# Performance work log

Hardware: AMD Instinct MI355X
Metric: run time of the kernel (lower is better)

## Reference

```python
import jax, jax.numpy as jnp
import numpy as np

NUM_NODES = 12
HEADS = 4
PERIOD = 24
HID = 144  # nn.LSTM(12*12, 12*12, 2)
NEG_INF = -9e15

ADJ = np.array([
    [1,0,0,0,0,1,0,0,0,0,1,1],
    [0,1,0,0,0,0,0,1,0,0,1,0],
    [0,0,1,0,0,0,1,0,0,0,0,1],
    [0,0,0,1,0,0,1,0,0,0,0,0],
    [0,0,0,0,1,1,0,0,0,0,0,0],
    [1,0,0,0,1,1,0,0,0,0,0,0],
    [0,0,1,1,0,0,1,0,0,0,1,0],
    [0,1,0,0,0,0,0,1,0,1,0,0],
    [0,0,0,0,0,0,0,0,1,1,1,1],
    [0,0,0,0,0,0,0,1,1,1,1,0],
    [1,1,0,0,0,0,1,0,1,1,1,1],
    [1,0,1,0,0,0,0,0,1,0,1,1]], dtype=np.int32)
EI, EJ = np.nonzero(ADJ)  # static edge list (row-major order, matches torch nonzero)


def gat_layer(x, W, b, a):
    # x: [B, N, c_in]; W: [c_in, H*c]; a: [H, 2c]
    B, N, _ = x.shape
    H = a.shape[0]
    h = (x @ W + b).reshape(B, N, H, -1)  # [B,N,H,c]
    # NOTE: adj has batch dim 1 in the original, so logits come from sample 0 only
    hi = h[0, EI]  # [E,H,c]
    hj = h[0, EJ]
    logits = jnp.einsum('ehc,hc->eh', jnp.concatenate([hi, hj], axis=-1), a)
    logits = jax.nn.leaky_relu(logits, 0.2)
    mat = jnp.full((N, N, H), NEG_INF, dtype=logits.dtype).at[EI, EJ].set(logits)
    probs = jax.nn.softmax(mat, axis=1)  # softmax over j (dim=2 in torch incl. batch)
    out = jnp.einsum('ijh,bjhc->bihc', probs, h)  # broadcast attn over batch
    return out.reshape(B, N, -1)  # concat heads


def lstm2(x, params, h0, c0):
    # x: [T,B,D]; params: list of (Wih,Whh,bih,bhh); h0,c0: [L,B,HID]
    hs, cs = [], []
    y = x
    for l, (Wih, Whh, bih, bhh) in enumerate(params):
        def step(carry, xt, Wih=Wih, Whh=Whh, bih=bih, bhh=bhh):
            h, c = carry
            g = xt @ Wih.T + h @ Whh.T + (bih + bhh)
            i, f, gg, o = jnp.split(g, 4, axis=-1)  # torch gate order i,f,g,o
            c2 = jax.nn.sigmoid(f) * c + jax.nn.sigmoid(i) * jnp.tanh(gg)
            h2 = jax.nn.sigmoid(o) * jnp.tanh(c2)
            return (h2, c2), h2
        (hT, cT), y = jax.lax.scan(step, (h0[l], c0[l]), y)
        hs.append(hT)
        cs.append(cT)
    return y, jnp.stack(hs), jnp.stack(cs)


def reference(x, gW0, gb0, ga0, gW1, gb1, ga1,
              eWih0, eWhh0, ebih0, ebhh0, eWih1, eWhh1, ebih1, ebhh1,
              dWih0, dWhh0, dbih0, dbhh0, dWih1, dWhh1, dbih1, dbhh1,
              gW3, gb3, ga3, gW4, gb4, ga4, fW, fb):
    B = x.shape[0]
    h = jax.nn.elu(gat_layer(x, gW0, gb0, ga0))           # [B,12,16]
    h = jax.nn.elu(gat_layer(h, gW1, gb1, ga1))           # [B,12,12]
    seq = h.reshape(PERIOD, -1, NUM_NODES * 12)            # [24, B/24, 144]
    Bb = seq.shape[1]
    z = jnp.zeros((2, Bb, HID), dtype=seq.dtype)
    enc_params = [(eWih0, eWhh0, ebih0, ebhh0), (eWih1, eWhh1, ebih1, ebhh1)]
    dec_params = [(dWih0, dWhh0, dbih0, dbhh0), (dWih1, dWhh1, dbih1, dbhh1)]
    y, hn, _ = lstm2(seq, enc_params, z, z)
    dec_in = jnp.zeros_like(y)
    y, _, _ = lstm2(dec_in, dec_params, hn, jnp.zeros_like(hn))
    h = y.reshape(-1, NUM_NODES, 12)                       # [B,12,12]
    h = jax.nn.elu(gat_layer(h, gW3, gb3, ga3))            # [B,12,16]
    h = jax.nn.elu(gat_layer(h, gW4, gb4, ga4))            # [B,12,24]
    h = h.reshape(B, NUM_NODES * 24)
    h = jax.nn.leaky_relu(h @ fW + fb, 0.01)               # fc_layers
    xr = h.reshape(B, NUM_NODES, -1)                       # [B,12,22]
    # F.mse_loss(..., reduce='sum') -> legacy truthy reduce => mean reduction
    out = jnp.mean((x - xr) ** 2, axis=(1, 2)).reshape(-1, 1)
    return out


def setup_inputs() -> dict:
    key = jax.random.key(0)
    ks = iter(jax.random.split(key, 64))
    def p(shape, s=0.2):
        return s * jax.random.normal(next(ks), shape, dtype=jnp.float32)
    B = 98304  # multiple of period=24
    d = {
        'x': jax.random.normal(next(ks), (B, 12, 22), dtype=jnp.float32),
        'gW0': p((22, 16)), 'gb0': p((16,)), 'ga0': p((4, 8)),
        'gW1': p((16, 12)), 'gb1': p((12,)), 'ga1': p((4, 6)),
    }
    for pre in ('e', 'd'):
        for l in (0, 1):
            d[f'{pre}Wih{l}'] = p((576, 144))
            d[f'{pre}Whh{l}'] = p((576, 144))
            d[f'{pre}bih{l}'] = p((576,))
            d[f'{pre}bhh{l}'] = p((576,))
    d.update({'gW3': p((12, 16)), 'gb3': p((16,)), 'ga3': p((4, 8)),
              'gW4': p((16, 24)), 'gb4': p((24,)), 'ga4': p((4, 12)),
              'fW': p((288, 264)), 'fb': p((264,))})
    return d
```

## Files before the change

### kernel.cpp

```cpp
#include <hip/hip_runtime.h>

#define DI __device__ __forceinline__

typedef short bfrag8 __attribute__((ext_vector_type(8)));
typedef float ffrag4 __attribute__((ext_vector_type(4)));

DI ushort f2b(float f){
  union { float f; unsigned u; } v; v.f = f;
  unsigned u = v.u;
  u += 0x7FFF + ((u >> 16) & 1);
  return (ushort)(u >> 16);
}
DI float b2f(ushort h){
  union { unsigned u; float f; } v; v.u = ((unsigned)h) << 16;
  return v.f;
}
DI float sigm(float x){ return 1.0f / (1.0f + __expf(-x)); }
DI float tanh_(float x){ return 1.0f - 2.0f / (1.0f + __expf(2.0f * x)); }
DI float elu_(float x){ return x > 0.f ? x : __expf(x) - 1.f; }

__global__ void k_probs(const float* xf, const ushort* xb, int in_c,
                        const float* W1, const float* b1, const float* a1, int hc1, int c1,
                        const float* W2, const float* b2, const float* a2, int hc2, int c2,
                        float* outA, float* outB)
{
  __shared__ float xs[12 * 22];
  __shared__ float h1[12 * 16];
  __shared__ float lg[4 * 144];
  __shared__ float pr[4 * 144];
  __shared__ float h1e[12 * 16];
  __shared__ float h2[12 * 24];
  const int t = threadIdx.x;
  const unsigned adj[12] = {0xC21u,0x482u,0x844u,0x048u,0x030u,0x031u,
                            0x44Cu,0x282u,0xF00u,0x780u,0xF43u,0xD05u};
  if (t < 12 * in_c){
    if (xf) xs[t] = xf[t];
    else    xs[t] = b2f(xb[t]);
  }
  __syncthreads();
  if (t < 12 * hc1){
    int i = t / hc1, o = t % hc1;
    float v = b1[o];
    for (int k = 0; k < in_c; k++) v += xs[i * in_c + k] * W1[k * hc1 + o];
    h1[t] = v;
  }
  __syncthreads();
  {
    int h = t / 144, ij = t % 144, i = ij / 12, j = ij % 12;
    float v;
    if ((adj[i] >> j) & 1){
      v = 0.f;
      for (int c = 0; c < c1; c++)
        v += a1[h*2*c1 + c] * h1[i*hc1 + h*c1 + c] + a1[h*2*c1 + c1 + c] * h1[j*hc1 + h*c1 + c];
      v = v > 0.f ? v : 0.2f * v;
    } else v = -9e15f;
    lg[t] = v;
  }
  __syncthreads();
  if (t < 48){
    int h = t / 12, i = t % 12;
    const float* row = &lg[h*144 + i*12];
    float m = row[0];
    for (int j = 1; j < 12; j++) m = fmaxf(m, row[j]);
    float e[12], s = 0.f;
    for (int j = 0; j < 12; j++){ e[j] = __expf(row[j] - m); s += e[j]; }
    float inv = 1.f / s;
    for (int j = 0; j < 12; j++){
      float p = e[j] * inv;
      pr[h*144 + i*12 + j] = p;
      outA[h*144 + i*12 + j] = p;
    }
  }
  __syncthreads();
  if (t < 12 * hc1){
    int i = t / hc1, o = t % hc1, h = o / c1;
    float v = 0.f;
    for (int j = 0; j < 12; j++) v += pr[h*144 + i*12 + j] * h1[j*hc1 + o];
    h1e[t] = elu_(v);
  }
  __syncthreads();
  if (t < 12 * hc2){
    int i = t / hc2, o = t % hc2;
    float v = b2[o];
    for (int k = 0; k < hc1; k++) v += h1e[i*hc1 + k] * W2[k*hc2 + o];
    h2[t] = v;
  }
  __syncthreads();
  {
    int h = t / 144, ij = t % 144, i = ij / 12, j = ij % 12;
    float v;
    if ((adj[i] >> j) & 1){
      v = 0.f;
      for (int c = 0; c < c2; c++)
        v += a2[h*2*c2 + c] * h2[i*hc2 + h*c2 + c] + a2[h*2*c2 + c2 + c] * h2[j*hc2 + h*c2 + c];
      v = v > 0.f ? v : 0.2f * v;
    } else v = -9e15f;
    lg[t] = v;
  }
  __syncthreads();
  if (t < 48){
    int h = t / 12, i = t % 12;
    const float* row = &lg[h*144 + i*12];
    float m = row[0];
    for (int j = 1; j < 12; j++) m = fmaxf(m, row[j]);
    float e[12], s = 0.f;
    for (int j = 0; j < 12; j++){ e[j] = __expf(row[j] - m); s += e[j]; }
    float inv = 1.f / s;
    for (int j = 0; j < 12; j++) outB[h*144 + i*12 + j] = e[j] * inv;
  }
}

__global__ void k_prep_op(const float* __restrict__ W, const float* __restrict__ p,
                          int Cin, int Cout, int hdiv, int K, int KT, int N,
                          ushort* __restrict__ dst)
{
  int bI = blockIdx.x;
  int kt = bI % KT, nt = bI / KT;
  int l = threadIdx.x, ln = l & 15, q = l >> 4;
  int n = nt * 16 + ln;
  for (int j = 0; j < 8; j++){
    int k = kt * 32 + q * 8 + j;
    float v = 0.f;
    if (k < K && n < N){
      if (p){
        int jj = k / Cin, kk = k % Cin;
        int i = n / Cout, o = n % Cout;
        v = p[(o / hdiv) * 144 + i * 12 + jj] * W[kk * Cout + o];
      } else {
        v = W[k * Cout + n];
      }
    }
    dst[((long)bI * 64 + l) * 8 + j] = f2b(v);
  }
}

__global__ void k_prep_lstm(const float* eWih0, const float* eWhh0,
                            const float* eWih1, const float* eWhh1,
                            const float* dWhh0,
                            const float* dWih1, const float* dWhh1,
                            ushort* __restrict__ dstBase)
{
  int combo = blockIdx.y;
  const float* Wh; const float* Wx; long off; int ntau;
  if (combo == 0){ Wh = eWhh0; Wx = eWih0; off = 0;      ntau = 72; }
  else if (combo == 1){ Wh = eWhh1; Wx = eWih1; off = 184320; ntau = 72; }
  else if (combo == 2){ Wh = dWhh0; Wx = dWhh0; off = 368640; ntau = 36; }
  else { Wh = dWhh1; Wx = dWih1; off = 460800; ntau = 72; }
  int bI = blockIdx.x;
  int tau = bI / 5, kt = bI % 5;
  if (tau >= ntau) return;
  const float* W = (tau < 36) ? Wh : Wx;
  int tt = (tau < 36) ? tau : tau - 36;
  int gt = tt / 9, ct = tt % 9;
  int l = threadIdx.x, ln = l & 15, q = l >> 4;
  int n = gt * 144 + ct * 16 + ln;
  ushort* d = dstBase + off;
  for (int j = 0; j < 8; j++){
    int k = kt * 32 + q * 8 + j;
    float v = (k < 144) ? W[(long)n * 144 + k] : 0.f;
    d[((long)bI * 64 + l) * 8 + j] = f2b(v);
  }
}

__global__ __launch_bounds__(512) void k_gat01(
    const float* __restrict__ x, const ushort* __restrict__ M0f, const float* __restrict__ b0,
    const ushort* __restrict__ M1f, const float* __restrict__ b1,
    ushort* __restrict__ seq)
{
  __shared__ ushort xs[128 * 288];
  __shared__ ushort h1e[128 * 200];
  int t = threadIdx.x;
  long row0 = (long)blockIdx.x * 128;
  int w = t >> 6, l = t & 63, q = l >> 4, ln = l & 15;
  if (t < 384){
    int row = t / 3, seg = t % 3;
    *(uint4*)&xs[row * 288 + 264 + seg * 8] = make_uint4(0u, 0u, 0u, 0u);
  }
  for (int idx = t; idx < 8448; idx += 512){
    int row = idx / 66, c4 = idx % 66;
    float4 v = *(const float4*)&x[(row0 + row) * 264 + c4 * 4];
    ushort4 o; o.x = f2b(v.x); o.y = f2b(v.y); o.z = f2b(v.z); o.w = f2b(v.w);
    *(ushort4*)&xs[row * 288 + c4 * 4] = o;
  }
  int nta[2] = {w, (w < 4) ? 8 + w : -1};
  bfrag8 f0[2][9];
  #pragma unroll
  for (int ii = 0; ii < 2; ii++)
    if (nta[ii] >= 0)
      #pragma unroll
      for (int kt = 0; kt < 9; kt++)
        f0[ii][kt] = *(const bfrag8*)&M0f[((long)(nta[ii] * 9 + kt) * 64 + l) * 8];
  float bias0 = b0[ln];
  __syncthreads();
  for (int rb = 0; rb < 8; rb++){
    bfrag8 af[9];
    #pragma unroll
    for (int kt = 0; kt < 9; kt++)
      af[kt] = *(const bfrag8*)&xs[(rb * 16 + ln) * 288 + kt * 32 + q * 8];
    #pragma unroll
    for (int ii = 0; ii < 2; ii++){
      if (nta[ii] < 0) continue;
      ffrag4 acc = {bias0, bias0, bias0, bias0};
      #pragma unroll
      for (int kt = 0; kt < 9; kt++)
        acc = __builtin_amdgcn_mfma_f32_16x16x32_bf16(af[kt], f0[ii][kt], acc, 0, 0, 0);
      #pragma unroll
      for (int r = 0; r < 4; r++)
        h1e[(rb * 16 + q * 4 + r) * 200 + nta[ii] * 16 + ln] = f2b(elu_(acc[r]));
    }
  }
  int ntb[2] = {w, (w == 0) ? 8 : -1};
  bfrag8 f1[2][6];
  #pragma unroll
  for (int ii = 0; ii < 2; ii++)
    if (ntb[ii] >= 0)
      #pragma unroll
      for (int kt = 0; kt < 6; kt++)
        f1[ii][kt] = *(const bfrag8*)&M1f[((long)(ntb[ii] * 6 + kt) * 64 + l) * 8];
  __syncthreads();
  for (int rb = 0; rb < 8; rb++){
    bfrag8 af[6];
    #pragma unroll
    for (int kt = 0; kt < 6; kt++)
      af[kt] = *(const bfrag8*)&h1e[(rb * 16 + ln) * 200 + kt * 32 + q * 8];
    #pragma unroll
    for (int ii = 0; ii < 2; ii++){
      if (ntb[ii] < 0) continue;
      int n = ntb[ii] * 16 + ln;
      float bias = b1[n % 12];
      ffrag4 acc = {bias, bias, bias, bias};
      #pragma unroll
      for (int kt = 0; kt < 6; kt++)
        acc = __builtin_amdgcn_mfma_f32_16x16x32_bf16(af[kt], f1[ii][kt], acc, 0, 0, 0);
      #pragma unroll
      for (int r = 0; r < 4; r++)
        xs[(rb * 16 + q * 4 + r) * 144 + n] = f2b(elu_(acc[r]));
    }
  }
  __syncthreads();
  for (int i = t; i < 2304; i += 512)
    *(uint4*)&seq[row0 * 144 + (long)i * 8] = *(uint4*)&xs[i * 8];
}

template<bool HASX>
__global__ __launch_bounds__(512, 2) void k_scan(
    const ushort* __restrict__ Wf,
    const ushort* __restrict__ seqin,
    const float* __restrict__ bih, const float* __restrict__ bhh,
    const ushort* __restrict__ h0,
    ushort* __restrict__ Y,
    ushort* __restrict__ hT)
{
  __shared__ float Px[2][11520];
  __shared__ float P8[1280];
  __shared__ ushort hl[2][2688];
  int t = threadIdx.x, rbk = blockIdx.x;
  int w = t >> 6, l = t & 63, q = l >> 4, ln = l & 15;
  if (t < 336){
    int row = t / 21, ch = t % 21;
    uint4 z = make_uint4(0u, 0u, 0u, 0u);
    if (h0 && ch < 18) z = *(const uint4*)&h0[((long)rbk * 16 + row) * 144 + ch * 8];
    *(uint4*)&hl[0][row * 168 + ch * 8] = z;
    *(uint4*)&hl[1][row * 168 + ch * 8] = make_uint4(0u, 0u, 0u, 0u);
  }
  if (w < 4){
    bfrag8 wh[2][4][5], w8[5];
    #pragma unroll
    for (int ci = 0; ci < 2; ci++)
      #pragma unroll
      for (int gt = 0; gt < 4; gt++)
        #pragma unroll
        for (int kt = 0; kt < 5; kt++)
          wh[ci][gt][kt] = *(const bfrag8*)&Wf[((long)((gt * 9 + 2 * w + ci) * 5 + kt) * 64 + l) * 8];
    #pragma unroll
    for (int kt = 0; kt < 5; kt++)
      w8[kt] = *(const bfrag8*)&Wf[((long)((w * 9 + 8) * 5 + kt) * 64 + l) * 8];
    float cst[2][4] = {};
    float c8 = 0.f;
    __syncthreads();
    for (int ts = 0; ts < 24; ts++){
      int par = ts & 1;
      const ushort* hlr = &hl[par][0];
      ushort* hlw = &hl[par ^ 1][0];
      bfrag8 ah[5];
      #pragma unroll
      for (int kt = 0; kt < 5; kt++)
        ah[kt] = *(const bfrag8*)&hlr[ln * 168 + kt * 32 + q * 8];
      #pragma unroll
      for (int ci = 0; ci < 2; ci++){
        int ct = 2 * w + ci;
        ffrag4 acc[4];
        #pragma unroll
        for (int gt = 0; gt < 4; gt++)
          acc[gt] = *(ffrag4*)&Px[par][(gt * 144 + ct * 16 + ln) * 20 + q * 4];
        #pragma unroll
        for (int gt = 0; gt < 4; gt++)
          #pragma unroll
          for (int kt = 0; kt < 5; kt++)
            acc[gt] = __builtin_amdgcn_mfma_f32_16x16x32_bf16(ah[kt], wh[ci][gt][kt], acc[gt], 0, 0, 0);
        #pragma unroll
        for (int r = 0; r < 4; r++){
          float cn = sigm(acc[1][r]) * cst[ci][r] + sigm(acc[0][r]) * tanh_(acc[2][r]);
          cst[ci][r] = cn;
          ushort hb = f2b(sigm(acc[3][r]) * tanh_(cn));
          hlw[(q * 4 + r) * 168 + ct * 16 + ln] = hb;
          if (Y) Y[(((long)ts * 4096) + rbk * 16 + q * 4 + r) * 144 + ct * 16 + ln] = hb;
        }
      }
      {
        ffrag4 a8 = *(ffrag4*)&Px[par][(w * 144 + 128 + ln) * 20 + q * 4];
        #pragma unroll
        for (int kt = 0; kt < 5; kt++)
          a8 = __builtin_amdgcn_mfma_f32_16x16x32_bf16(ah[kt], w8[kt], a8, 0, 0, 0);
        *(ffrag4*)&P8[(w * 16 + ln) * 20 + q * 4] = a8;
      }
      __syncthreads();
      if (t < 256){
        int row = t >> 4, c8c = t & 15;
        float iv = P8[(0 * 16 + c8c) * 20 + row];
        float fv = P8[(1 * 16 + c8c) * 20 + row];
        float gv = P8[(2 * 16 + c8c) * 20 + row];
        float ov = P8[(3 * 16 + c8c) * 20 + row];
        float cn = sigm(fv) * c8 + sigm(iv) * tanh_(gv);
        c8 = cn;
        ushort hb = f2b(sigm(ov) * tanh_(cn));
        hl[par ^ 1][row * 168 + 128 + c8c] = hb;
        if (Y) Y[(((long)ts * 4096) + rbk * 16 + row) * 144 + 128 + c8c] = hb;
      }
      __syncthreads();
    }
  } else {
    int j = w - 4;
    bfrag8 wx[9][5];
    float biasx[9];
    #pragma unroll
    for (int i = 0; i < 9; i++){
      int n = j * 144 + i * 16 + ln;
      biasx[i] = bih[n] + bhh[n];
      if (HASX)
        #pragma unroll
        for (int kt = 0; kt < 5; kt++)
          wx[i][kt] = *(const bfrag8*)&Wf[((long)((36 + j * 9 + i) * 5 + kt) * 64 + l) * 8];
    }
    bfrag8 axc[5];
    if (HASX){
      const ushort* xr = &seqin[((long)rbk * 16 + ln) * 144];
      #pragma unroll
      for (int kt = 0; kt < 5; kt++)
        axc[kt] = *(const bfrag8*)&xr[kt * 32 + q * 8];
      #pragma unroll
      for (int i = 0; i < 9; i++){
        ffrag4 acc = {biasx[i], biasx[i], biasx[i], biasx[i]};
        #pragma unroll
        for (int kt = 0; kt < 5; kt++)
          acc = __builtin_amdgcn_mfma_f32_16x16x32_bf16(axc[kt], wx[i][kt], acc, 0, 0, 0);
        *(ffrag4*)&Px[0][(j * 144 + i * 16 + ln) * 20 + q * 4] = acc;
      }
      const ushort* xr1 = &seqin[(4096L + (long)rbk * 16 + ln) * 144];
      #pragma unroll
      for (int kt = 0; kt < 5; kt++)
        axc[kt] = *(const bfrag8*)&xr1[kt * 32 + q * 8];
    } else {
      #pragma unroll
      for (int i = 0; i < 9; i++){
        ffrag4 acc = {biasx[i], biasx[i], biasx[i], biasx[i]};
        *(ffrag4*)&Px[0][(j * 144 + i * 16 + ln) * 20 + q * 4] = acc;
        *(ffrag4*)&Px[1][(j * 144 + i * 16 + ln) * 20 + q * 4] = acc;
      }
    }
    __syncthreads();
    for (int ts = 0; ts < 24; ts++){
      if (HASX && ts < 23){
        int par = ts & 1;
        #pragma unroll
        for (int i = 0; i < 9; i++){
          ffrag4 acc = {biasx[i], biasx[i], biasx[i], biasx[i]};
          #pragma unroll
          for (int kt = 0; kt < 5; kt++)
            acc = __builtin_amdgcn_mfma_f32_16x16x32_bf16(axc[kt], wx[i][kt], acc, 0, 0, 0);
          *(ffrag4*)&Px[par ^ 1][(j * 144 + i * 16 + ln) * 20 + q * 4] = acc;
        }
        if (ts < 22){
          const ushort* xr = &seqin[(((long)(ts + 2)) * 4096 + (long)rbk * 16 + ln) * 144];
          #pragma unroll
          for (int kt = 0; kt < 5; kt++)
            axc[kt] = *(const bfrag8*)&xr[kt * 32 + q * 8];
        }
      }
      __syncthreads();
      __syncthreads();
    }
  }
  if (hT && t < 288){
    int row = t / 18, ch = t % 18;
    *(uint4*)&hT[((long)rbk * 16 + row) * 144 + ch * 8] = *(uint4*)&hl[0][row * 168 + ch * 8];
  }
}

__global__ __launch_bounds__(512) void k_tail(
    const ushort* __restrict__ Ya, const ushort* __restrict__ M3f, const float* __restrict__ b3,
    const ushort* __restrict__ M4f, const float* __restrict__ b4,
    const ushort* __restrict__ fWt, const float* __restrict__ fb,
    const float* __restrict__ x, float* __restrict__ out)
{
  __shared__ ushort h3e[128 * 200];
  __shared__ ushort bufB[128 * 288];
  __shared__ float psum[128 * 8];
  ushort* ys = bufB;
  ushort* h4e = bufB;
  int t = threadIdx.x;
  long row0 = (long)blockIdx.x * 128;
  int w = t >> 6, l = t & 63, q = l >> 4, ln = l & 15;
  if (t < 256){
    int row = t / 2, seg = t % 2;
    *(uint4*)&ys[row * 160 + 144 + seg * 8] = make_uint4(0u, 0u, 0u, 0u);
  }
  for (int idx = t; idx < 2304; idx += 512){
    int row = idx / 18, ch = idx % 18;
    *(uint4*)&ys[row * 160 + ch * 8] = *(const uint4*)&Ya[(row0 + row) * 144 + (long)ch * 8];
  }
  int nta[2] = {w, (w < 4) ? 8 + w : -1};
  bfrag8 f3[2][5];
  #pragma unroll
  for (int ii = 0; ii < 2; ii++)
    if (nta[ii] >= 0)
      #pragma unroll
      for (int kt = 0; kt < 5; kt++)
        f3[ii][kt] = *(const bfrag8*)&M3f[((long)(nta[ii] * 5 + kt) * 64 + l) * 8];
  float bias3 = b3[ln];
  __syncthreads();
  for (int rb = 0; rb < 8; rb++){
    bfrag8 af[5];
    #pragma unroll
    for (int kt = 0; kt < 5; kt++)
      af[kt] = *(const bfrag8*)&ys[(rb * 16 + ln) * 160 + kt * 32 + q * 8];
    #pragma unroll
    for (int ii = 0; ii < 2; ii++){
      if (nta[ii] < 0) continue;
      ffrag4 acc = {bias3, bias3, bias3, bias3};
      #pragma unroll
      for (int kt = 0; kt < 5; kt++)
        acc = __builtin_amdgcn_mfma_f32_16x16x32_bf16(af[kt], f3[ii][kt], acc, 0, 0, 0);
      #pragma unroll
      for (int r = 0; r < 4; r++)
        h3e[(rb * 16 + q * 4 + r) * 200 + nta[ii] * 16 + ln] = f2b(elu_(acc[r]));
    }
  }
  int ntb[3] = {2 * w, 2 * w + 1, (w < 2) ? 16 + w : -1};
  bfrag8 f4[3][6];
  #pragma unroll
  for (int ii = 0; ii < 3; ii++)
    if (ntb[ii] >= 0)
      #pragma unroll
      for (int kt = 0; kt < 6; kt++)
        f4[ii][kt] = *(const bfrag8*)&M4f[((long)(ntb[ii] * 6 + kt) * 64 + l) * 8];
  __syncthreads();
  for (int rb = 0; rb < 8; rb++){
    bfrag8 af[6];
    #pragma unroll
    for (int kt = 0; kt < 6; kt++)
      af[kt] = *(const bfrag8*)&h3e[(rb * 16 + ln) * 200 + kt * 32 + q * 8];
    #pragma unroll
    for (int ii = 0; ii < 3; ii++){
      if (ntb[ii] < 0) continue;
      int n = ntb[ii] * 16 + ln;
      float bias = b4[n % 24];
      ffrag4 acc = {bias, bias, bias, bias};
      #pragma unroll
      for (int kt = 0; kt < 6; kt++)
        acc = __builtin_amdgcn_mfma_f32_16x16x32_bf16(af[kt], f4[ii][kt], acc, 0, 0, 0);
      #pragma unroll
      for (int r = 0; r < 4; r++)
        h4e[(rb * 16 + q * 4 + r) * 288 + n] = f2b(elu_(acc[r]));
    }
  }
  int ntc[3] = {2 * w, 2 * w + 1, (w == 0) ? 16 : -1};
  bfrag8 f5[3][9];
  float bias5[3] = {0.f, 0.f, 0.f};
  #pragma unroll
  for (int ii = 0; ii < 3; ii++)
    if (ntc[ii] >= 0){
      #pragma unroll
      for (int kt = 0; kt < 9; kt++)
        f5[ii][kt] = *(const bfrag8*)&fWt[((long)(ntc[ii] * 9 + kt) * 64 + l) * 8];
      int n = ntc[ii] * 16 + ln;
      bias5[ii] = (n < 264) ? fb[n] : 0.f;
    }
  __syncthreads();
  for (int rb = 0; rb < 8; rb++){
    bfrag8 af[9];
    #pragma unroll
    for (int kt = 0; kt < 9; kt++)
      af[kt] = *(const bfrag8*)&h4e[(rb * 16 + ln) * 288 + kt * 32 + q * 8];
    float s4[4] = {0.f, 0.f, 0.f, 0.f};
    #pragma unroll
    for (int ii = 0; ii < 3; ii++){
      if (ntc[ii] < 0) continue;
      ffrag4 acc = {bias5[ii], bias5[ii], bias5[ii], bias5[ii]};
      #pragma unroll
      for (int kt = 0; kt < 9; kt++)
        acc = __builtin_amdgcn_mfma_f32_16x16x32_bf16(af[kt], f5[ii][kt], acc, 0, 0, 0);
      int n = ntc[ii] * 16 + ln;
      if (n < 264){
        #pragma unroll
        for (int r = 0; r < 4; r++){
          float v = acc[r];
          v = v > 0.f ? v : 0.01f * v;
          long row = row0 + rb * 16 + q * 4 + r;
          float d = x[row * 264 + n] - v;
          s4[r] += d * d;
        }
      }
    }
    #pragma unroll
    for (int off = 1; off < 16; off <<= 1){
      #pragma unroll
      for (int r = 0; r < 4; r++) s4[r] += __shfl_xor(s4[r], off, 16);
    }
    if (ln == 0){
      #pragma unroll
      for (int r = 0; r < 4; r++) psum[(rb * 16 + q * 4 + r) * 8 + w] = s4[r];
    }
  }
  __syncthreads();
  if (t < 128){
    float s = 0.f;
    for (int k = 0; k < 8; k++) s += psum[t * 8 + k];
    out[row0 + t] = s * (1.0f / 264.0f);
  }
}

extern "C" void kernel_launch(void* const* d_in, const int* in_sizes, int n_in,
                              void* d_out, int out_size, void* d_ws, size_t ws_size,
                              hipStream_t stream)
{
  const float* x     = (const float*)d_in[0];
  const float* gW0   = (const float*)d_in[1];
  const float* gb0   = (const float*)d_in[2];
  const float* ga0   = (const float*)d_in[3];
  const float* gW1   = (const float*)d_in[4];
  const float* gb1   = (const float*)d_in[5];
  const float* ga1   = (const float*)d_in[6];
  const float* eWih0 = (const float*)d_in[7];
  const float* eWhh0 = (const float*)d_in[8];
  const float* ebih0 = (const float*)d_in[9];
  const float* ebhh0 = (const float*)d_in[10];
  const float* eWih1 = (const float*)d_in[11];
  const float* eWhh1 = (const float*)d_in[12];
  const float* ebih1 = (const float*)d_in[13];
  const float* ebhh1 = (const float*)d_in[14];
  const float* dWhh0 = (const float*)d_in[16];
  const float* dbih0 = (const float*)d_in[17];
  const float* dbhh0 = (const float*)d_in[18];
  const float* dWih1 = (const float*)d_in[19];
  const float* dWhh1 = (const float*)d_in[20];
  const float* dbih1 = (const float*)d_in[21];
  const float* dbhh1 = (const float*)d_in[22];
  const float* gW3   = (const float*)d_in[23];
  const float* gb3   = (const float*)d_in[24];
  const float* ga3   = (const float*)d_in[25];
  const float* gW4   = (const float*)d_in[26];
  const float* gb4   = (const float*)d_in[27];
  const float* ga4   = (const float*)d_in[28];
  const float* fW    = (const float*)d_in[29];
  const float* fb    = (const float*)d_in[30];

  char* ws = (char*)d_ws;
  float*  probs0 = (float*)(ws + 0);
  float*  probs1 = (float*)(ws + 2304);
  float*  probs3 = (float*)(ws + 4608);
  float*  probs4 = (float*)(ws + 6912);
  ushort* M0f    = (ushort*)(ws + 9216);
  ushort* M1f    = (ushort*)(ws + 119808);
  ushort* M3f    = (ushort*)(ws + 175104);
  ushort* M4f    = (ushort*)(ws + 236544);
  ushort* fWt    = (ushort*)(ws + 347136);
  ushort* lstmF  = (ushort*)(ws + 503808);
  ushort* seq    = (ushort*)(ws + 1794048);
  ushort* Ya     = (ushort*)(ws + 30105600);
  ushort* Yb     = (ushort*)(ws + 58417152);
  ushort* hT0    = (ushort*)(ws + 86728704);
  ushort* hT1    = (ushort*)(ws + 87908352);
  float* out = (float*)d_out;

  k_prep_lstm<<<dim3(360, 4), 64, 0, stream>>>(eWih0, eWhh0, eWih1, eWhh1,
                                               dWhh0, dWih1, dWhh1, lstmF);
  k_prep_op<<<153, 64, 0, stream>>>(fW, nullptr, 0, 264, 1, 288, 9, 264, fWt);
  k_probs<<<1, 576, 0, stream>>>(x, nullptr, 22,
                                 gW0, gb0, ga0, 16, 4,
                                 gW1, gb1, ga1, 12, 3,
                                 probs0, probs1);
  k_prep_op<<<108, 64, 0, stream>>>(gW0, probs0, 22, 16, 4, 264, 9, 192, M0f);
  k_prep_op<<<54, 64, 0, stream>>>(gW1, probs1, 16, 12, 3, 192, 6, 144, M1f);
  k_gat01<<<768, 512, 0, stream>>>(x, M0f, gb0, M1f, gb1, seq);

  k_scan<true><<<256, 512, 0, stream>>>(lstmF + 0L,      seq, ebih0, ebhh0, nullptr, Ya, hT0);
  k_scan<true><<<256, 512, 0, stream>>>(lstmF + 184320L, Ya, ebih1, ebhh1, nullptr, nullptr, hT1);
  k_scan<false><<<256, 512, 0, stream>>>(lstmF + 368640L, nullptr, dbih0, dbhh0, hT0, Yb, nullptr);
  k_scan<true><<<256, 512, 0, stream>>>(lstmF + 460800L, Yb, dbih1, dbhh1, hT1, Ya, nullptr);

  k_probs<<<1, 576, 0, stream>>>(nullptr, Ya, 12,
                                 gW3, gb3, ga3, 16, 4,
                                 gW4, gb4, ga4, 24, 6,
                                 probs3, probs4);
  k_prep_op<<<60, 64, 0, stream>>>(gW3, probs3, 12, 16, 4, 144, 5, 192, M3f);
  k_prep_op<<<108, 64, 0, stream>>>(gW4, probs4, 16, 24, 6, 192, 6, 288, M4f);
  k_tail<<<768, 512, 0, stream>>>(Ya, M3f, gb3, M4f, gb4, fWt, fb, x, out);
}
```

Measured before the change: 598.2 us.

## Fuse weight prep into fewer kernels, halve GAT tiles, restructure LSTM scan

Merges the LSTM and FC weight-prep kernels into one launch, and folds the GAT operator-matrix construction into k_probs, removing several small launches. The GAT head and tail kernels now process 64 rows per block (twice the blocks) with padded LDS strides to improve occupancy and reduce bank conflicts. The LSTM scan is reorganized so four waves compute all hidden-gate MFMAs into a shared Ph buffer while the other waves prefetch input projections, and all 512 threads then do the elementwise cell update and write Y with vectorized stores. This costs more LDS traffic and an extra barrier per timestep in exchange for spreading the gate math across all threads.

```diff
diff --git a/kernel.cpp b/kernel.cpp
--- a/kernel.cpp
+++ b/kernel.cpp
@@ -22,12 +22,14 @@
 __global__ void k_probs(const float* xf, const ushort* xb, int in_c,
                         const float* W1, const float* b1, const float* a1, int hc1, int c1,
                         const float* W2, const float* b2, const float* a2, int hc2, int c2,
-                        float* outA, float* outB)
+                        ushort* __restrict__ M1dst, int KT1,
+                        ushort* __restrict__ M2dst, int KT2)
 {
   __shared__ float xs[12 * 22];
   __shared__ float h1[12 * 16];
-  __shared__ float lg[4 * 144];
-  __shared__ float pr[4 * 144];
+  __shared__ float lg[576];
+  __shared__ float prA[576];
+  __shared__ float prB[576];
   __shared__ float h1e[12 * 16];
   __shared__ float h2[12 * 24];
   const int t = threadIdx.x;
@@ -65,17 +67,13 @@
     float e[12], s = 0.f;
     for (int j = 0; j < 12; j++){ e[j] = __expf(row[j] - m); s += e[j]; }
     float inv = 1.f / s;
-    for (int j = 0; j < 12; j++){
-      float p = e[j] * inv;
-      pr[h*144 + i*12 + j] = p;
-      outA[h*144 + i*12 + j] = p;
-    }
+    for (int j = 0; j < 12; j++) prA[h*144 + i*12 + j] = e[j] * inv;
   }
   __syncthreads();
   if (t < 12 * hc1){
     int i = t / hc1, o = t % hc1, h = o / c1;
     float v = 0.f;
-    for (int j = 0; j < 12; j++) v += pr[h*144 + i*12 + j] * h1[j*hc1 + o];
+    for (int j = 0; j < 12; j++) v += prA[h*144 + i*12 + j] * h1[j*hc1 + o];
     h1e[t] = elu_(v);
   }
   __syncthreads();
@@ -106,45 +104,81 @@
     float e[12], s = 0.f;
     for (int j = 0; j < 12; j++){ e[j] = __expf(row[j] - m); s += e[j]; }
     float inv = 1.f / s;
-    for (int j = 0; j < 12; j++) outB[h*144 + i*12 + j] = e[j] * inv;
-  }
-}
-
-__global__ void k_prep_op(const float* __restrict__ W, const float* __restrict__ p,
-                          int Cin, int Cout, int hdiv, int K, int KT, int N,
-                          ushort* __restrict__ dst)
+    for (int j = 0; j < 12; j++) prB[h*144 + i*12 + j] = e[j] * inv;
+  }
+  __syncthreads();
+  {
+    int NT = (12 * hc1) / 16, K = 12 * in_c;
+    for (int idx = t; idx < NT * KT1 * 64; idx += 576){
+      int bI = idx >> 6, li = idx & 63;
+      int kt = bI % KT1, nt = bI / KT1;
+      int n = nt * 16 + (li & 15);
+      int i = n / hc1, o = n % hc1;
+      union { ushort u[8]; uint4 v; } pk;
+      #pragma unroll
+      for (int j = 0; j < 8; j++){
+        int k = kt * 32 + (li >> 4) * 8 + j;
+        float v = 0.f;
+        if (k < K){
+          int jj = k / in_c, kk = k % in_c;
+          v = prA[(o / c1) * 144 + i * 12 + jj] * W1[kk * hc1 + o];
+        }
+        pk.u[j] = f2b(v);
+      }
+      *(uint4*)&M1dst[(long)idx * 8] = pk.v;
+    }
+  }
+  {
+    int NT = (12 * hc2) / 16, K = 12 * hc1;
+    for (int idx = t; idx < NT * KT2 * 64; idx += 576){
+      int bI = idx >> 6, li = idx & 63;
+      int kt = bI % KT2, nt = bI / KT2;
+      int n = nt * 16 + (li & 15);
+      int i = n / hc2, o = n % hc2;
+      union { ushort u[8]; uint4 v; } pk;
+      #pragma unroll
+      for (int j = 0; j < 8; j++){
+        int k = kt * 32 + (li >> 4) * 8 + j;
+        float v = 0.f;
+        if (k < K){
+          int jj = k / hc1, kk = k % hc1;
+          v = prB[(o / c2) * 144 + i * 12 + jj] * W2[kk * hc2 + o];
+        }
+        pk.u[j] = f2b(v);
+      }
+      *(uint4*)&M2dst[(long)idx * 8] = pk.v;
+    }
+  }
+}
+
+__global__ void k_prep_all(const float* eWih0, const float* eWhh0,
+                           const float* eWih1, const float* eWhh1,
+                           const float* dWhh0,
+                           const float* dWih1, const float* dWhh1,
+                           const float* fW,
+                           ushort* __restrict__ lstmF, ushort* __restrict__ fWt)
 {
-  int bI = blockIdx.x;
-  int kt = bI % KT, nt = bI / KT;
+  int y = blockIdx.y;
   int l = threadIdx.x, ln = l & 15, q = l >> 4;
-  int n = nt * 16 + ln;
-  for (int j = 0; j < 8; j++){
-    int k = kt * 32 + q * 8 + j;
-    float v = 0.f;
-    if (k < K && n < N){
-      if (p){
-        int jj = k / Cin, kk = k % Cin;
-        int i = n / Cout, o = n % Cout;
-        v = p[(o / hdiv) * 144 + i * 12 + jj] * W[kk * Cout + o];
-      } else {
-        v = W[k * Cout + n];
-      }
-    }
-    dst[((long)bI * 64 + l) * 8 + j] = f2b(v);
-  }
-}
-
-__global__ void k_prep_lstm(const float* eWih0, const float* eWhh0,
-                            const float* eWih1, const float* eWhh1,
-                            const float* dWhh0,
-                            const float* dWih1, const float* dWhh1,
-                            ushort* __restrict__ dstBase)
-{
-  int combo = blockIdx.y;
+  if (y == 4){
+    int bI = blockIdx.x;
+    if (bI >= 153) return;
+    int nt = bI / 9, kt = bI % 9;
+    int n = nt * 16 + ln;
+    union { ushort u[8]; uint4 v; } pk;
+    #pragma unroll
+    for (int j = 0; j < 8; j++){
+      int k = kt * 32 + q * 8 + j;
+      float v = (k < 288 && n < 264) ? fW[k * 264 + n] : 0.f;
+      pk.u[j] = f2b(v);
+    }
+    *(uint4*)&fWt[((long)(bI * 64 + l)) * 8] = pk.v;
+    return;
+  }
   const float* Wh; const float* Wx; long off; int ntau;
-  if (combo == 0){ Wh = eWhh0; Wx = eWih0; off = 0;      ntau = 72; }
-  else if (combo == 1){ Wh = eWhh1; Wx = eWih1; off = 184320; ntau = 72; }
-  else if (combo == 2){ Wh = dWhh0; Wx = dWhh0; off = 368640; ntau = 36; }
+  if (y == 0){ Wh = eWhh0; Wx = eWih0; off = 0;      ntau = 72; }
+  else if (y == 1){ Wh = eWhh1; Wx = eWih1; off = 184320; ntau = 72; }
+  else if (y == 2){ Wh = dWhh0; Wx = dWhh0; off = 368640; ntau = 36; }
   else { Wh = dWhh1; Wx = dWih1; off = 460800; ntau = 72; }
   int bI = blockIdx.x;
   int tau = bI / 5, kt = bI % 5;
@@ -152,14 +186,16 @@
   const float* W = (tau < 36) ? Wh : Wx;
   int tt = (tau < 36) ? tau : tau - 36;
   int gt = tt / 9, ct = tt % 9;
-  int l = threadIdx.x, ln = l & 15, q = l >> 4;
   int n = gt * 144 + ct * 16 + ln;
-  ushort* d = dstBase + off;
+  ushort* d = lstmF + off;
+  union { ushort u[8]; uint4 v; } pk;
+  #pragma unroll
   for (int j = 0; j < 8; j++){
     int k = kt * 32 + q * 8 + j;
     float v = (k < 144) ? W[(long)n * 144 + k] : 0.f;
-    d[((long)bI * 64 + l) * 8 + j] = f2b(v);
-  }
+    pk.u[j] = f2b(v);
+  }
+  *(uint4*)&d[((long)(bI * 64 + l)) * 8] = pk.v;
 }
 
 __global__ __launch_bounds__(512) void k_gat01(
@@ -167,20 +203,20 @@
     const ushort* __restrict__ M1f, const float* __restrict__ b1,
     ushort* __restrict__ seq)
 {
-  __shared__ ushort xs[128 * 288];
-  __shared__ ushort h1e[128 * 200];
+  __shared__ ushort xs[64 * 296];
+  __shared__ ushort h1e[64 * 200];
   int t = threadIdx.x;
-  long row0 = (long)blockIdx.x * 128;
+  long row0 = (long)blockIdx.x * 64;
   int w = t >> 6, l = t & 63, q = l >> 4, ln = l & 15;
-  if (t < 384){
-    int row = t / 3, seg = t % 3;
-    *(uint4*)&xs[row * 288 + 264 + seg * 8] = make_uint4(0u, 0u, 0u, 0u);
-  }
-  for (int idx = t; idx < 8448; idx += 512){
+  if (t < 256){
+    int row = t >> 2, seg = t & 3;
+    *(uint4*)&xs[row * 296 + 264 + seg * 8] = make_uint4(0u, 0u, 0u, 0u);
+  }
+  for (int idx = t; idx < 4224; idx += 512){
     int row = idx / 66, c4 = idx % 66;
     float4 v = *(const float4*)&x[(row0 + row) * 264 + c4 * 4];
     ushort4 o; o.x = f2b(v.x); o.y = f2b(v.y); o.z = f2b(v.z); o.w = f2b(v.w);
-    *(ushort4*)&xs[row * 288 + c4 * 4] = o;
+    *(ushort4*)&xs[row * 296 + c4 * 4] = o;
   }
   int nta[2] = {w, (w < 4) ? 8 + w : -1};
   bfrag8 f0[2][9];
@@ -192,11 +228,11 @@
         f0[ii][kt] = *(const bfrag8*)&M0f[((long)(nta[ii] * 9 + kt) * 64 + l) * 8];
   float bias0 = b0[ln];
   __syncthreads();
-  for (int rb = 0; rb < 8; rb++){
+  for (int rb = 0; rb < 4; rb++){
     bfrag8 af[9];
     #pragma unroll
     for (int kt = 0; kt < 9; kt++)
-      af[kt] = *(const bfrag8*)&xs[(rb * 16 + ln) * 288 + kt * 32 + q * 8];
+      af[kt] = *(const bfrag8*)&xs[(rb * 16 + ln) * 296 + kt * 32 + q * 8];
     #pragma unroll
     for (int ii = 0; ii < 2; ii++){
       if (nta[ii] < 0) continue;
@@ -218,7 +254,7 @@
       for (int kt = 0; kt < 6; kt++)
         f1[ii][kt] = *(const bfrag8*)&M1f[((long)(ntb[ii] * 6 + kt) * 64 + l) * 8];
   __syncthreads();
-  for (int rb = 0; rb < 8; rb++){
+  for (int rb = 0; rb < 4; rb++){
     bfrag8 af[6];
     #pragma unroll
     for (int kt = 0; kt < 6; kt++)
@@ -238,7 +274,7 @@
     }
   }
   __syncthreads();
-  for (int i = t; i < 2304; i += 512)
+  for (int i = t; i < 1152; i += 512)
     *(uint4*)&seq[row0 * 144 + (long)i * 8] = *(uint4*)&xs[i * 8];
 }
 
@@ -251,98 +287,38 @@
     ushort* __restrict__ Y,
     ushort* __restrict__ hT)
 {
+  __shared__ float Ph[11520];
   __shared__ float Px[2][11520];
-  __shared__ float P8[1280];
   __shared__ ushort hl[2][2688];
   int t = threadIdx.x, rbk = blockIdx.x;
   int w = t >> 6, l = t & 63, q = l >> 4, ln = l & 15;
   if (t < 336){
     int row = t / 21, ch = t % 21;
     uint4 z = make_uint4(0u, 0u, 0u, 0u);
+    *(uint4*)&hl[1][row * 168 + ch * 8] = z;
     if (h0 && ch < 18) z = *(const uint4*)&h0[((long)rbk * 16 + row) * 144 + ch * 8];
     *(uint4*)&hl[0][row * 168 + ch * 8] = z;
-    *(uint4*)&hl[1][row * 168 + ch * 8] = make_uint4(0u, 0u, 0u, 0u);
-  }
-  if (w < 4){
-    bfrag8 wh[2][4][5], w8[5];
-    #pragma unroll
-    for (int ci = 0; ci < 2; ci++)
-      #pragma unroll
-      for (int gt = 0; gt < 4; gt++)
-        #pragma unroll
-        for (int kt = 0; kt < 5; kt++)
-          wh[ci][gt][kt] = *(const bfrag8*)&Wf[((long)((gt * 9 + 2 * w + ci) * 5 + kt) * 64 + l) * 8];
-    #pragma unroll
-    for (int kt = 0; kt < 5; kt++)
-      w8[kt] = *(const bfrag8*)&Wf[((long)((w * 9 + 8) * 5 + kt) * 64 + l) * 8];
-    float cst[2][4] = {};
-    float c8 = 0.f;
-    __syncthreads();
-    for (int ts = 0; ts < 24; ts++){
-      int par = ts & 1;
-      const ushort* hlr = &hl[par][0];
-      ushort* hlw = &hl[par ^ 1][0];
-      bfrag8 ah[5];
+  }
+  bool isH = (w < 4);
+  bfrag8 wf[9][5];
+  if (HASX || isH){
+    #pragma unroll
+    for (int i = 0; i < 9; i++){
+      int tau = isH ? (w * 9 + i) : (36 + (w - 4) * 9 + i);
       #pragma unroll
       for (int kt = 0; kt < 5; kt++)
-        ah[kt] = *(const bfrag8*)&hlr[ln * 168 + kt * 32 + q * 8];
-      #pragma unroll
-      for (int ci = 0; ci < 2; ci++){
-        int ct = 2 * w + ci;
-        ffrag4 acc[4];
-        #pragma unroll
-        for (int gt = 0; gt < 4; gt++)
-          acc[gt] = *(ffrag4*)&Px[par][(gt * 144 + ct * 16 + ln) * 20 + q * 4];
-        #pragma unroll
-        for (int gt = 0; gt < 4; gt++)
-          #pragma unroll
-          for (int kt = 0; kt < 5; kt++)
-            acc[gt] = __builtin_amdgcn_mfma_f32_16x16x32_bf16(ah[kt], wh[ci][gt][kt], acc[gt], 0, 0, 0);
-        #pragma unroll
-        for (int r = 0; r < 4; r++){
-          float cn = sigm(acc[1][r]) * cst[ci][r] + sigm(acc[0][r]) * tanh_(acc[2][r]);
-          cst[ci][r] = cn;
-          ushort hb = f2b(sigm(acc[3][r]) * tanh_(cn));
-          hlw[(q * 4 + r) * 168 + ct * 16 + ln] = hb;
-          if (Y) Y[(((long)ts * 4096) + rbk * 16 + q * 4 + r) * 144 + ct * 16 + ln] = hb;
-        }
-      }
-      {
-        ffrag4 a8 = *(ffrag4*)&Px[par][(w * 144 + 128 + ln) * 20 + q * 4];
-        #pragma unroll
-        for (int kt = 0; kt < 5; kt++)
-          a8 = __builtin_amdgcn_mfma_f32_16x16x32_bf16(ah[kt], w8[kt], a8, 0, 0, 0);
-        *(ffrag4*)&P8[(w * 16 + ln) * 20 + q * 4] = a8;
-      }
-      __syncthreads();
-      if (t < 256){
-        int row = t >> 4, c8c = t & 15;
-        float iv = P8[(0 * 16 + c8c) * 20 + row];
-        float fv = P8[(1 * 16 + c8c) * 20 + row];
-        float gv = P8[(2 * 16 + c8c) * 20 + row];
-        float ov = P8[(3 * 16 + c8c) * 20 + row];
-        float cn = sigm(fv) * c8 + sigm(iv) * tanh_(gv);
-        c8 = cn;
-        ushort hb = f2b(sigm(ov) * tanh_(cn));
-        hl[par ^ 1][row * 168 + 128 + c8c] = hb;
-        if (Y) Y[(((long)ts * 4096) + rbk * 16 + row) * 144 + 128 + c8c] = hb;
-      }
-      __syncthreads();
-    }
-  } else {
-    int j = w - 4;
-    bfrag8 wx[9][5];
-    float biasx[9];
+        wf[i][kt] = *(const bfrag8*)&Wf[((long)(tau * 5 + kt) * 64 + l) * 8];
+    }
+  }
+  float cst[5] = {0.f, 0.f, 0.f, 0.f, 0.f};
+  float biasx[9];
+  bfrag8 axc[5];
+  if (!isH){
     #pragma unroll
     for (int i = 0; i < 9; i++){
-      int n = j * 144 + i * 16 + ln;
+      int n = ((w - 4) * 9 + i) * 16 + ln;
       biasx[i] = bih[n] + bhh[n];
-      if (HASX)
-        #pragma unroll
-        for (int kt = 0; kt < 5; kt++)
-          wx[i][kt] = *(const bfrag8*)&Wf[((long)((36 + j * 9 + i) * 5 + kt) * 64 + l) * 8];
-    }
-    bfrag8 axc[5];
+    }
     if (HASX){
       const ushort* xr = &seqin[((long)rbk * 16 + ln) * 144];
       #pragma unroll
@@ -353,8 +329,8 @@
         ffrag4 acc = {biasx[i], biasx[i], biasx[i], biasx[i]};
         #pragma unroll
         for (int kt = 0; kt < 5; kt++)
-          acc = __builtin_amdgcn_mfma_f32_16x16x32_bf16(axc[kt], wx[i][kt], acc, 0, 0, 0);
-        *(ffrag4*)&Px[0][(j * 144 + i * 16 + ln) * 20 + q * 4] = acc;
+          acc = __builtin_amdgcn_mfma_f32_16x16x32_bf16(axc[kt], wf[i][kt], acc, 0, 0, 0);
+        *(ffrag4*)&Px[0][(((w - 4) * 9 + i) * 16 + ln) * 20 + q * 4] = acc;
       }
       const ushort* xr1 = &seqin[(4096L + (long)rbk * 16 + ln) * 144];
       #pragma unroll
@@ -364,31 +340,64 @@
       #pragma unroll
       for (int i = 0; i < 9; i++){
         ffrag4 acc = {biasx[i], biasx[i], biasx[i], biasx[i]};
-        *(ffrag4*)&Px[0][(j * 144 + i * 16 + ln) * 20 + q * 4] = acc;
-        *(ffrag4*)&Px[1][(j * 144 + i * 16 + ln) * 20 + q * 4] = acc;
+        *(ffrag4*)&Px[0][(((w - 4) * 9 + i) * 16 + ln) * 20 + q * 4] = acc;
+        *(ffrag4*)&Px[1][(((w - 4) * 9 + i) * 16 + ln) * 20 + q * 4] = acc;
+      }
+    }
+  }
+  __syncthreads();
+  for (int ts = 0; ts < 24; ts++){
+    int par = ts & 1;
+    if (isH){
+      bfrag8 ah[5];
+      #pragma unroll
+      for (int kt = 0; kt < 5; kt++)
+        ah[kt] = *(const bfrag8*)&hl[par][ln * 168 + kt * 32 + q * 8];
+      #pragma unroll
+      for (int i = 0; i < 9; i++){
+        ffrag4 acc = {0.f, 0.f, 0.f, 0.f};
+        #pragma unroll
+        for (int kt = 0; kt < 5; kt++)
+          acc = __builtin_amdgcn_mfma_f32_16x16x32_bf16(ah[kt], wf[i][kt], acc, 0, 0, 0);
+        *(ffrag4*)&Ph[((w * 9 + i) * 16 + ln) * 20 + q * 4] = acc;
+      }
+    } else if (HASX && ts < 23){
+      #pragma unroll
+      for (int i = 0; i < 9; i++){
+        ffrag4 acc = {biasx[i], biasx[i], biasx[i], biasx[i]};
+        #pragma unroll
+        for (int kt = 0; kt < 5; kt++)
+          acc = __builtin_amdgcn_mfma_f32_16x16x32_bf16(axc[kt], wf[i][kt], acc, 0, 0, 0);
+        *(ffrag4*)&Px[par ^ 1][(((w - 4) * 9 + i) * 16 + ln) * 20 + q * 4] = acc;
+      }
+      if (ts < 22){
+        const ushort* xr = &seqin[(((long)(ts + 2)) * 4096 + (long)rbk * 16 + ln) * 144];
+        #pragma unroll
+        for (int kt = 0; kt < 5; kt++)
+          axc[kt] = *(const bfrag8*)&xr[kt * 32 + q * 8];
       }
     }
     __syncthreads();
-    for (int ts = 0; ts < 24; ts++){
-      if (HASX && ts < 23){
-        int par = ts & 1;
-        #pragma unroll
-        for (int i = 0; i < 9; i++){
-          ffrag4 acc = {biasx[i], biasx[i], biasx[i], biasx[i]};
-          #pragma unroll
-          for (int kt = 0; kt < 5; kt++)
-            acc = __builtin_amdgcn_mfma_f32_16x16x32_bf16(axc[kt], wx[i][kt], acc, 0, 0, 0);
-          *(ffrag4*)&Px[par ^ 1][(j * 144 + i * 16 + ln) * 20 + q * 4] = acc;
-        }
-        if (ts < 22){
-          const ushort* xr = &seqin[(((long)(ts + 2)) * 4096 + (long)rbk * 16 + ln) * 144];
-          #pragma unroll
-          for (int kt = 0; kt < 5; kt++)
-            axc[kt] = *(const bfrag8*)&xr[kt * 32 + q * 8];
-        }
-      }
-      __syncthreads();
-      __syncthreads();
+    #pragma unroll
+    for (int j = 0; j < 5; j++){
+      int cell = j * 512 + t;
+      if (cell < 2304){
+        int col = cell >> 4, row = cell & 15;
+        int a = col * 20 + row;
+        float iv = Ph[a]        + Px[par][a];
+        float fv = Ph[2880 + a] + Px[par][2880 + a];
+        float gv = Ph[5760 + a] + Px[par][5760 + a];
+        float ov = Ph[8640 + a] + Px[par][8640 + a];
+        float cn = sigm(fv) * cst[j] + sigm(iv) * tanh_(gv);
+        cst[j] = cn;
+        hl[par ^ 1][row * 168 + col] = f2b(sigm(ov) * tanh_(cn));
+      }
+    }
+    __syncthreads();
+    if (Y && t < 288){
+      int row = t / 18, ch = t % 18;
+      *(uint4*)&Y[(((long)ts * 4096) + rbk * 16 + row) * 144 + ch * 8] =
+          *(uint4*)&hl[par ^ 1][row * 168 + ch * 8];
     }
   }
   if (hT && t < 288){
@@ -403,21 +412,21 @@
     const ushort* __restrict__ fWt, const float* __restrict__ fb,
     const float* __restrict__ x, float* __restrict__ out)
 {
-  __shared__ ushort h3e[128 * 200];
-  __shared__ ushort bufB[128 * 288];
-  __shared__ float psum[128 * 8];
+  __shared__ ushort h3e[64 * 200];
+  __shared__ ushort bufB[64 * 296];
+  __shared__ float psum[64 * 8];
   ushort* ys = bufB;
   ushort* h4e = bufB;
   int t = threadIdx.x;
-  long row0 = (long)blockIdx.x * 128;
+  long row0 = (long)blockIdx.x * 64;
   int w = t >> 6, l = t & 63, q = l >> 4, ln = l & 15;
-  if (t < 256){
-    int row = t / 2, seg = t % 2;
-    *(uint4*)&ys[row * 160 + 144 + seg * 8] = make_uint4(0u, 0u, 0u, 0u);
-  }
-  for (int idx = t; idx < 2304; idx += 512){
+  if (t < 192){
+    int row = t / 3, seg = t % 3;
+    *(uint4*)&ys[row * 168 + 144 + seg * 8] = make_uint4(0u, 0u, 0u, 0u);
+  }
+  for (int idx = t; idx < 1152; idx += 512){
     int row = idx / 18, ch = idx % 18;
-    *(uint4*)&ys[row * 160 + ch * 8] = *(const uint4*)&Ya[(row0 + row) * 144 + (long)ch * 8];
+    *(uint4*)&ys[row * 168 + ch * 8] = *(const uint4*)&Ya[(row0 + row) * 144 + (long)ch * 8];
   }
   int nta[2] = {w, (w < 4) ? 8 + w : -1};
   bfrag8 f3[2][5];
@@ -429,11 +438,11 @@
         f3[ii][kt] = *(const bfrag8*)&M3f[((long)(nta[ii] * 5 + kt) * 64 + l) * 8];
   float bias3 = b3[ln];
   __syncthreads();
-  for (int rb = 0; rb < 8; rb++){
+  for (int rb = 0; rb < 4; rb++){
     bfrag8 af[5];
     #pragma unroll
     for (int kt = 0; kt < 5; kt++)
-      af[kt] = *(const bfrag8*)&ys[(rb * 16 + ln) * 160 + kt * 32 + q * 8];
+      af[kt] = *(const bfrag8*)&ys[(rb * 16 + ln) * 168 + kt * 32 + q * 8];
     #pragma unroll
     for (int ii = 0; ii < 2; ii++){
       if (nta[ii] < 0) continue;
@@ -455,7 +464,7 @@
       for (int kt = 0; kt < 6; kt++)
         f4[ii][kt] = *(const bfrag8*)&M4f[((long)(ntb[ii] * 6 + kt) * 64 + l) * 8];
   __syncthreads();
-  for (int rb = 0; rb < 8; rb++){
+  for (int rb = 0; rb < 4; rb++){
     bfrag8 af[6];
     #pragma unroll
     for (int kt = 0; kt < 6; kt++)
@@ -471,7 +480,7 @@
         acc = __builtin_amdgcn_mfma_f32_16x16x32_bf16(af[kt], f4[ii][kt], acc, 0, 0, 0);
       #pragma unroll
       for (int r = 0; r < 4; r++)
-        h4e[(rb * 16 + q * 4 + r) * 288 + n] = f2b(elu_(acc[r]));
+        h4e[(rb * 16 + q * 4 + r) * 296 + n] = f2b(elu_(acc[r]));
     }
   }
   int ntc[3] = {2 * w, 2 * w + 1, (w == 0) ? 16 : -1};
@@ -487,11 +496,11 @@
       bias5[ii] = (n < 264) ? fb[n] : 0.f;
     }
   __syncthreads();
-  for (int rb = 0; rb < 8; rb++){
+  for (int rb = 0; rb < 4; rb++){
     bfrag8 af[9];
     #pragma unroll
     for (int kt = 0; kt < 9; kt++)
-      af[kt] = *(const bfrag8*)&h4e[(rb * 16 + ln) * 288 + kt * 32 + q * 8];
+      af[kt] = *(const bfrag8*)&h4e[(rb * 16 + ln) * 296 + kt * 32 + q * 8];
     float s4[4] = {0.f, 0.f, 0.f, 0.f};
     #pragma unroll
     for (int ii = 0; ii < 3; ii++){
@@ -523,7 +532,7 @@
     }
   }
   __syncthreads();
-  if (t < 128){
+  if (t < 64){
     float s = 0.f;
     for (int k = 0; k < 8; k++) s += psum[t * 8 + k];
     out[row0 + t] = s * (1.0f / 264.0f);
@@ -566,10 +575,6 @@
   const float* fb    = (const float*)d_in[30];
 
   char* ws = (char*)d_ws;
-  float*  probs0 = (float*)(ws + 0);
-  float*  probs1 = (float*)(ws + 2304);
-  float*  probs3 = (float*)(ws + 4608);
-  float*  probs4 = (float*)(ws + 6912);
   ushort* M0f    = (ushort*)(ws + 9216);
   ushort* M1f    = (ushort*)(ws + 119808);
   ushort* M3f    = (ushort*)(ws + 175104);
@@ -583,16 +588,13 @@
   ushort* hT1    = (ushort*)(ws + 87908352);
   float* out = (float*)d_out;
 
-  k_prep_lstm<<<dim3(360, 4), 64, 0, stream>>>(eWih0, eWhh0, eWih1, eWhh1,
-                                               dWhh0, dWih1, dWhh1, lstmF);
-  k_prep_op<<<153, 64, 0, stream>>>(fW, nullptr, 0, 264, 1, 288, 9, 264, fWt);
+  k_prep_all<<<dim3(360, 5), 64, 0, stream>>>(eWih0, eWhh0, eWih1, eWhh1,
+                                              dWhh0, dWih1, dWhh1, fW, lstmF, fWt);
   k_probs<<<1, 576, 0, stream>>>(x, nullptr, 22,
                                  gW0, gb0, ga0, 16, 4,
                                  gW1, gb1, ga1, 12, 3,
-                                 probs0, probs1);
-  k_prep_op<<<108, 64, 0, stream>>>(gW0, probs0, 22, 16, 4, 264, 9, 192, M0f);
-  k_prep_op<<<54, 64, 0, stream>>>(gW1, probs1, 16, 12, 3, 192, 6, 144, M1f);
-  k_gat01<<<768, 512, 0, stream>>>(x, M0f, gb0, M1f, gb1, seq);
+                                 M0f, 9, M1f, 6);
+  k_gat01<<<1536, 512, 0, stream>>>(x, M0f, gb0, M1f, gb1, seq);
 
   k_scan<true><<<256, 512, 0, stream>>>(lstmF + 0L,      seq, ebih0, ebhh0, nullptr, Ya, hT0);
   k_scan<true><<<256, 512, 0, stream>>>(lstmF + 184320L, Ya, ebih1, ebhh1, nullptr, nullptr, hT1);
@@ -602,8 +604,6 @@
   k_probs<<<1, 576, 0, stream>>>(nullptr, Ya, 12,
                                  gW3, gb3, ga3, 16, 4,
                                  gW4, gb4, ga4, 24, 6,
-                                 probs3, probs4);
-  k_prep_op<<<60, 64, 0, stream>>>(gW3, probs3, 12, 16, 4, 144, 5, 192, M3f);
-  k_prep_op<<<108, 64, 0, stream>>>(gW4, probs4, 16, 24, 6, 192, 6, 288, M4f);
-  k_tail<<<768, 512, 0, stream>>>(Ya, M3f, gb3, M4f, gb4, fWt, fb, x, out);
-}
+                                 M3f, 5, M4f, 6);
+  k_tail<<<1536, 512, 0, stream>>>(Ya, M3f, gb3, M4f, gb4, fWt, fb, x, out);
+}
```

New measurement: 859.0 us. 1.44x slower.
